# Kernel tuning notes

Measured on AMD Instinct MI355X. Metric: run time of the kernel, lower is better.

The kernel has to match this reference:

```python
import jax, jax.numpy as jnp
import numpy as np

HIDDEN = 51
N, T = 1024, 2048


def _uinit(key, shape, fan):
    bound = 1.0 / np.sqrt(fan)
    return jax.random.uniform(key, shape, jnp.float32, -bound, bound)


def setup_inputs() -> dict:
    key = jax.random.key(0)
    ks = jax.random.split(key, 9)
    H = HIDDEN
    return {
        "stimulus": jax.random.normal(ks[0], (N, T), jnp.float32),
        # layer 1: LSTMCell(input=1, hidden=H); torch gate order [i, f, g, o]
        "W_ih1": _uinit(ks[1], (4 * H, 1), H),
        "W_hh1": _uinit(ks[2], (4 * H, H), H),
        "b_ih1": _uinit(ks[3], (4 * H,), H),
        "b_hh1": _uinit(ks[4], (4 * H,), H),
        # layer 2: LSTMCell(input=H, hidden=1)
        "W_ih2": _uinit(ks[5], (4, H), 1),
        "W_hh2": _uinit(ks[6], (4, 1), 1),
        "b_ih2": _uinit(ks[7], (4,), 1),
        "b_hh2": _uinit(ks[8], (4,), 1),
    }


def _lstm_cell(x, h, c, W_ih, W_hh, b_ih, b_hh):
    # x: (N, in), h/c: (N, H). torch LSTMCell math, gate order i,f,g,o.
    gates = x @ W_ih.T + h @ W_hh.T + b_ih + b_hh  # (N, 4H)
    i, f, g, o = jnp.split(gates, 4, axis=-1)
    c_new = jax.nn.sigmoid(f) * c + jax.nn.sigmoid(i) * jnp.tanh(g)
    h_new = jax.nn.sigmoid(o) * jnp.tanh(c_new)
    return h_new, c_new


def reference(stimulus, W_ih1, W_hh1, b_ih1, b_hh1, W_ih2, W_hh2, b_ih2, b_hh2):
    n, t = stimulus.shape
    H = W_hh1.shape[1]
    h1 = jnp.zeros((n, H), stimulus.dtype)
    c1 = jnp.zeros((n, H), stimulus.dtype)
    h2 = jnp.zeros((n, 1), stimulus.dtype)
    c2 = jnp.zeros((n, 1), stimulus.dtype)

    def step(carry, x_t):  # x_t: (N,)
        h1, c1, h2, c2 = carry
        h1, c1 = _lstm_cell(x_t[:, None], h1, c1, W_ih1, W_hh1, b_ih1, b_hh1)
        h2, c2 = _lstm_cell(h1, h2, c2, W_ih2, W_hh2, b_ih2, b_hh2)
        return (h1, c1, h2, c2), h2[:, 0]

    _, ys = jax.lax.scan(step, (h1, c1, h2, c2), stimulus.T)  # ys: (T, N)
    return ys.T  # (N, T)
```

## Files before the change

### kernel.cpp

```cpp
#include <hip/hip_runtime.h>


constexpr int H  = 51;
constexpr int TL = 2048;

typedef float v2f __attribute__((ext_vector_type(2)));

__device__ __forceinline__ float rcpf(float x)   { return __builtin_amdgcn_rcpf(x); }
__device__ __forceinline__ float exp2f_(float x) { return __builtin_amdgcn_exp2f(x); }

constexpr float LOG2E  = 1.442695041f;
constexpr float LOG2E2 = 2.885390082f;

template <int CTRL>
__device__ __forceinline__ float dppmov(float v) {
    return __int_as_float(__builtin_amdgcn_update_dpp(
        0, __float_as_int(v), CTRL, 0xF, 0xF, true));
}

__device__ __forceinline__ float wave_sum(float p) {
    p += dppmov<0xB1>(p);
    p += dppmov<0x4E>(p);
    p += dppmov<0x124>(p);
    p += dppmov<0x128>(p);
    p += __int_as_float(__builtin_amdgcn_ds_swizzle(__float_as_int(p), 0x401f));
    p += __shfl_xor(p, 32, 64);
    return p;
}

template <int PAT>
__device__ __forceinline__ float quadb(float v) {
    return __int_as_float(__builtin_amdgcn_update_dpp(
        0, __float_as_int(v), PAT, 0xF, 0xF, true));
}

__device__ __forceinline__ void pk_fma(v2f& acc, const v2f a, const v2f b) {
    asm("v_pk_fma_f32 %0, %1, %2, %0" : "+v"(acc) : "v"(a), "v"(b));
}

__device__ __forceinline__ void layer2_step(
    const float* __restrict__ hprev, int lane,
    const float4& w2, const float4& wh2, const float4& b2,
    float* __restrict__ c2h2, float* __restrict__ out_ptr)
{
    const float hp = (lane < H) ? hprev[lane] : 0.0f;
    const float p0 = wave_sum(w2.x * hp);
    const float p1 = wave_sum(w2.y * hp);
    const float p2 = wave_sum(w2.z * hp);
    const float p3 = wave_sum(w2.w * hp);
    const float c2 = c2h2[0], h2 = c2h2[1];
    const float a0 = fmaf(wh2.x, h2, p0) + b2.x;
    const float a1 = fmaf(wh2.y, h2, p1) + b2.y;
    const float a2 = fmaf(wh2.z, h2, p2) + b2.z;
    const float a3 = fmaf(wh2.w, h2, p3) + b2.w;
    const float si = rcpf(1.0f + exp2f_(a0 * -LOG2E));
    const float sf = rcpf(1.0f + exp2f_(a1 * -LOG2E));
    const float tg = 1.0f - 2.0f * rcpf(1.0f + exp2f_(a2 * LOG2E2));
    const float so = rcpf(1.0f + exp2f_(a3 * -LOG2E));
    const float c2n = fmaf(sf, c2, si * tg);
    const float h2n = so * (1.0f - 2.0f * rcpf(1.0f + exp2f_(c2n * LOG2E2)));
    if (lane == 0) { c2h2[0] = c2n; c2h2[1] = h2n; *out_ptr = h2n; }
}

__global__ void
__attribute__((amdgpu_flat_work_group_size(256, 256)))
__attribute__((amdgpu_waves_per_eu(4, 4)))
lstm2_fused(const float* __restrict__ stim,
            const float* __restrict__ Wih1,
            const float* __restrict__ Whh1,
            const float* __restrict__ bih1,
            const float* __restrict__ bhh1,
            const float* __restrict__ Wih2,
            const float* __restrict__ Whh2,
            const float* __restrict__ bih2,
            const float* __restrict__ bhh2,
            float* __restrict__ out)
{
    const int n    = blockIdx.x;
    const int tid  = threadIdx.x;
    const int wid  = tid >> 6;
    const int lane = tid & 63;
    const int gate = lane & 3;
    const int unit = wid * 16 + (lane >> 2);
    const bool uval = (unit < H);

    __shared__ __align__(16) float xrow[TL];
    __shared__ __align__(16) float hbuf[2][56];
    __shared__ float c2h2[2];

    {
        const float4* s4 = reinterpret_cast<const float4*>(stim + (size_t)n * TL);
        float4* d4 = reinterpret_cast<float4*>(xrow);
        d4[tid]       = s4[tid];
        d4[tid + 256] = s4[tid + 256];
    }

    v2f wa0, wb0, wa1, wb1, wa2, wb2, wa3, wb3, wa4, wb4, wa5, wb5,
        wa6, wb6, wa7, wb7, wa8, wb8, wa9, wb9, wa10, wb10, wa11, wb11,
        wa12, wb12;
    float bsum = 0.0f, wi1 = 0.0f;
    {
        const v2f z = {0.0f, 0.0f};
        wa0=z; wb0=z; wa1=z; wb1=z; wa2=z; wb2=z; wa3=z; wb3=z; wa4=z; wb4=z;
        wa5=z; wb5=z; wa6=z; wb6=z; wa7=z; wb7=z; wa8=z; wb8=z; wa9=z; wb9=z;
        wa10=z; wb10=z; wa11=z; wb11=z; wa12=z; wb12=z;
    }
    if (uval) {
        const int r = gate * H + unit;
        const float* wr = Whh1 + r * H;
        #define LDJ(J) wa##J = (v2f){wr[4*(J)+0], wr[4*(J)+1]}; \
                       wb##J = (v2f){wr[4*(J)+2], wr[4*(J)+3]};
        LDJ(0) LDJ(1) LDJ(2) LDJ(3) LDJ(4) LDJ(5)
        LDJ(6) LDJ(7) LDJ(8) LDJ(9) LDJ(10) LDJ(11)
        #undef LDJ
        wa12 = (v2f){wr[48], wr[49]};
        wb12 = (v2f){wr[50], 0.0f};
        bsum = bih1[r] + bhh1[r];
        wi1  = Wih1[r];
    }

    float4 w2c, wh2c, b2c;
    w2c = make_float4(
        (lane < H) ? Wih2[0 * H + lane] : 0.0f,
        (lane < H) ? Wih2[1 * H + lane] : 0.0f,
        (lane < H) ? Wih2[2 * H + lane] : 0.0f,
        (lane < H) ? Wih2[3 * H + lane] : 0.0f);
    wh2c = make_float4(Whh2[0], Whh2[1], Whh2[2], Whh2[3]);
    b2c  = make_float4(bih2[0] + bhh2[0], bih2[1] + bhh2[1],
                       bih2[2] + bhh2[2], bih2[3] + bhh2[3]);

    if (tid < 56) { hbuf[0][tid] = 0.0f; hbuf[1][tid] = 0.0f; }
    if (tid == 0) { c2h2[0] = 0.0f; c2h2[1] = 0.0f; }
    __syncthreads();

    float c1 = 0.0f;
    float* out_row = out + (size_t)n * TL;
    const int rot = (n + (n >> 8)) & 3;

    for (int t = 0; t < TL; ++t) {
        const float* hprev = hbuf[(t & 1) ^ 1];

        if (t > 0 && wid == ((t + rot) & 3)) {
            layer2_step(hprev, lane, w2c, wh2c, b2c, c2h2, out_row + (t - 1));
        }

        const float x = xrow[t];
        v2f acc0 = {fmaf(x, wi1, bsum), 0.0f};
        v2f acc1 = {0.0f, 0.0f};
        const float4* h4 = reinterpret_cast<const float4*>(hprev);
        #define DOT(J) { const float4 hv = h4[J]; \
            pk_fma(acc0, wa##J, (v2f){hv.x, hv.y}); \
            pk_fma(acc1, wb##J, (v2f){hv.z, hv.w}); }
        DOT(0) DOT(1) DOT(2) DOT(3) DOT(4) DOT(5)
        DOT(6) DOT(7) DOT(8) DOT(9) DOT(10) DOT(11) DOT(12)
        #undef DOT
        const float a = (acc0.x + acc1.x) + (acc0.y + acc1.y);

        const bool  istanh = (gate == 2);
        const float k  = istanh ? LOG2E2 : -LOG2E;
        const float rr = rcpf(1.0f + exp2f_(a * k));
        const float v  = istanh ? fmaf(-2.0f, rr, 1.0f) : rr;

        const float vi = quadb<0x00>(v);
        const float vf = quadb<0x55>(v);
        const float vg = quadb<0xAA>(v);
        const float vo = quadb<0xFF>(v);

        c1 = fmaf(vf, c1, vi * vg);
        const float h1 = vo * (1.0f - 2.0f * rcpf(1.0f + exp2f_(c1 * LOG2E2)));
        if (uval && gate == 0) hbuf[t & 1][unit] = h1;

        __syncthreads();
    }

    if (wid == ((TL + rot) & 3)) {
        layer2_step(hbuf[(TL & 1) ^ 1], lane, w2c, wh2c, b2c, c2h2, out_row + (TL - 1));
    }
}

extern "C" void kernel_launch(void* const* d_in, const int* in_sizes, int n_in,
                              void* d_out, int out_size, void* d_ws, size_t ws_size,
                              hipStream_t stream) {
    const float* stim = (const float*)d_in[0];
    const float* Wih1 = (const float*)d_in[1];
    const float* Whh1 = (const float*)d_in[2];
    const float* bih1 = (const float*)d_in[3];
    const float* bhh1 = (const float*)d_in[4];
    const float* Wih2 = (const float*)d_in[5];
    const float* Whh2 = (const float*)d_in[6];
    const float* bih2 = (const float*)d_in[7];
    const float* bhh2 = (const float*)d_in[8];
    float* out = (float*)d_out;

    const int N = in_sizes[0] / TL;
    lstm2_fused<<<dim3(N), dim3(256), 0, stream>>>(
        stim, Wih1, Whh1, bih1, bhh1, Wih2, Whh2, bih2, bhh2, out);
}
```

Baseline: 1.745 ms.

## Split each gate dot product across two lanes and double block size to 512

Each block now uses 8 waves, and each (unit, gate) row's 51-element recurrent dot product is split across two adjacent lanes, which are combined with a DPP swap. This roughly halves the serial FMA chain per step. Gate values are gathered with ds_swizzle across 8-lane groups, and the layer-2 step rotates across 8 waves. The cost is more waves competing per barrier, fewer resident blocks per CU, and swizzle latency on the critical path.

After: 2.484 ms. 42.3% more time.

```diff
diff --git a/kernel.cpp b/kernel.cpp
--- a/kernel.cpp
+++ b/kernel.cpp
@@ -5,6 +5,7 @@
 constexpr int TL = 2048;
 
 typedef float v2f __attribute__((ext_vector_type(2)));
+typedef float v4f __attribute__((ext_vector_type(4)));
 
 __device__ __forceinline__ float rcpf(float x)   { return __builtin_amdgcn_rcpf(x); }
 __device__ __forceinline__ float exp2f_(float x) { return __builtin_amdgcn_exp2f(x); }
@@ -18,20 +19,19 @@
         0, __float_as_int(v), CTRL, 0xF, 0xF, true));
 }
 
+template <int OFF>
+__device__ __forceinline__ float swzb(float v) {
+    return __int_as_float(__builtin_amdgcn_ds_swizzle(__float_as_int(v), OFF));
+}
+
 __device__ __forceinline__ float wave_sum(float p) {
     p += dppmov<0xB1>(p);
     p += dppmov<0x4E>(p);
     p += dppmov<0x124>(p);
     p += dppmov<0x128>(p);
-    p += __int_as_float(__builtin_amdgcn_ds_swizzle(__float_as_int(p), 0x401f));
+    p += swzb<0x401f>(p);
     p += __shfl_xor(p, 32, 64);
     return p;
-}
-
-template <int PAT>
-__device__ __forceinline__ float quadb(float v) {
-    return __int_as_float(__builtin_amdgcn_update_dpp(
-        0, __float_as_int(v), PAT, 0xF, 0xF, true));
 }
 
 __device__ __forceinline__ void pk_fma(v2f& acc, const v2f a, const v2f b) {
@@ -62,27 +62,27 @@
     if (lane == 0) { c2h2[0] = c2n; c2h2[1] = h2n; *out_ptr = h2n; }
 }
 
-__global__ void
-__attribute__((amdgpu_flat_work_group_size(256, 256)))
-__attribute__((amdgpu_waves_per_eu(4, 4)))
-lstm2_fused(const float* __restrict__ stim,
-            const float* __restrict__ Wih1,
-            const float* __restrict__ Whh1,
-            const float* __restrict__ bih1,
-            const float* __restrict__ bhh1,
-            const float* __restrict__ Wih2,
-            const float* __restrict__ Whh2,
-            const float* __restrict__ bih2,
-            const float* __restrict__ bhh2,
-            float* __restrict__ out)
+__global__ __launch_bounds__(512)
+void lstm2_fused(const float* __restrict__ stim,
+                 const float* __restrict__ Wih1,
+                 const float* __restrict__ Whh1,
+                 const float* __restrict__ bih1,
+                 const float* __restrict__ bhh1,
+                 const float* __restrict__ Wih2,
+                 const float* __restrict__ Whh2,
+                 const float* __restrict__ bih2,
+                 const float* __restrict__ bhh2,
+                 float* __restrict__ out)
 {
     const int n    = blockIdx.x;
     const int tid  = threadIdx.x;
     const int wid  = tid >> 6;
     const int lane = tid & 63;
-    const int gate = lane & 3;
-    const int unit = wid * 16 + (lane >> 2);
+    const int half = lane & 1;
+    const int gate = (lane >> 1) & 3;
+    const int unit = wid * 8 + (lane >> 3);
     const bool uval = (unit < H);
+    const int kb   = half * 28;
 
     __shared__ __align__(16) float xrow[TL];
     __shared__ __align__(16) float hbuf[2][56];
@@ -91,43 +91,31 @@
     {
         const float4* s4 = reinterpret_cast<const float4*>(stim + (size_t)n * TL);
         float4* d4 = reinterpret_cast<float4*>(xrow);
-        d4[tid]       = s4[tid];
-        d4[tid + 256] = s4[tid + 256];
+        d4[tid] = s4[tid];
     }
 
-    v2f wa0, wb0, wa1, wb1, wa2, wb2, wa3, wb3, wa4, wb4, wa5, wb5,
-        wa6, wb6, wa7, wb7, wa8, wb8, wa9, wb9, wa10, wb10, wa11, wb11,
-        wa12, wb12;
-    float bsum = 0.0f, wi1 = 0.0f;
-    {
-        const v2f z = {0.0f, 0.0f};
-        wa0=z; wb0=z; wa1=z; wb1=z; wa2=z; wb2=z; wa3=z; wb3=z; wa4=z; wb4=z;
-        wa5=z; wb5=z; wa6=z; wb6=z; wa7=z; wb7=z; wa8=z; wb8=z; wa9=z; wb9=z;
-        wa10=z; wb10=z; wa11=z; wb11=z; wa12=z; wb12=z;
-    }
-    if (uval) {
-        const int r = gate * H + unit;
-        const float* wr = Whh1 + r * H;
-        #define LDJ(J) wa##J = (v2f){wr[4*(J)+0], wr[4*(J)+1]}; \
-                       wb##J = (v2f){wr[4*(J)+2], wr[4*(J)+3]};
-        LDJ(0) LDJ(1) LDJ(2) LDJ(3) LDJ(4) LDJ(5)
-        LDJ(6) LDJ(7) LDJ(8) LDJ(9) LDJ(10) LDJ(11)
-        #undef LDJ
-        wa12 = (v2f){wr[48], wr[49]};
-        wb12 = (v2f){wr[50], 0.0f};
-        bsum = bih1[r] + bhh1[r];
-        wi1  = Wih1[r];
-    }
+    const int r = gate * H + unit;
+    const float* wr = Whh1 + (size_t)(uval ? r : 0) * H;
+    #define SELW(K) (((K) < H && uval) ? wr[((K) < H) ? (K) : 0] : 0.0f)
+    v2f wpa0, wpb0, wpa1, wpb1, wpa2, wpb2, wpa3, wpb3, wpa4, wpb4,
+        wpa5, wpb5, wpa6, wpb6;
+    #define LW(J) wpa##J = (v2f){SELW(kb+4*(J)+0), SELW(kb+4*(J)+1)}; \
+                  wpb##J = (v2f){SELW(kb+4*(J)+2), SELW(kb+4*(J)+3)};
+    LW(0) LW(1) LW(2) LW(3) LW(4) LW(5) LW(6)
+    #undef LW
+    #undef SELW
+    const float bsum = uval ? (bih1[r] + bhh1[r]) : 0.0f;
+    const float wi1  = uval ? Wih1[r] : 0.0f;
 
-    float4 w2c, wh2c, b2c;
-    w2c = make_float4(
-        (lane < H) ? Wih2[0 * H + lane] : 0.0f,
-        (lane < H) ? Wih2[1 * H + lane] : 0.0f,
-        (lane < H) ? Wih2[2 * H + lane] : 0.0f,
-        (lane < H) ? Wih2[3 * H + lane] : 0.0f);
-    wh2c = make_float4(Whh2[0], Whh2[1], Whh2[2], Whh2[3]);
-    b2c  = make_float4(bih2[0] + bhh2[0], bih2[1] + bhh2[1],
-                       bih2[2] + bhh2[2], bih2[3] + bhh2[3]);
+    const int lc = (lane < H) ? lane : 0;
+    float4 w2c = make_float4(
+        (lane < H) ? Wih2[0 * H + lc] : 0.0f,
+        (lane < H) ? Wih2[1 * H + lc] : 0.0f,
+        (lane < H) ? Wih2[2 * H + lc] : 0.0f,
+        (lane < H) ? Wih2[3 * H + lc] : 0.0f);
+    float4 wh2c = make_float4(Whh2[0], Whh2[1], Whh2[2], Whh2[3]);
+    float4 b2c  = make_float4(bih2[0] + bhh2[0], bih2[1] + bhh2[1],
+                              bih2[2] + bhh2[2], bih2[3] + bhh2[3]);
 
     if (tid < 56) { hbuf[0][tid] = 0.0f; hbuf[1][tid] = 0.0f; }
     if (tid == 0) { c2h2[0] = 0.0f; c2h2[1] = 0.0f; }
@@ -135,45 +123,48 @@
 
     float c1 = 0.0f;
     float* out_row = out + (size_t)n * TL;
-    const int rot = (n + (n >> 8)) & 3;
+    const int rot = (n + (n >> 8)) & 7;
 
     for (int t = 0; t < TL; ++t) {
         const float* hprev = hbuf[(t & 1) ^ 1];
 
-        if (t > 0 && wid == ((t + rot) & 3)) {
+        if (t > 0 && wid == ((t + rot) & 7)) {
             layer2_step(hprev, lane, w2c, wh2c, b2c, c2h2, out_row + (t - 1));
         }
 
         const float x = xrow[t];
-        v2f acc0 = {fmaf(x, wi1, bsum), 0.0f};
+        const float* hp = hprev + kb;
+        v2f acc0 = {0.0f, 0.0f};
         v2f acc1 = {0.0f, 0.0f};
-        const float4* h4 = reinterpret_cast<const float4*>(hprev);
-        #define DOT(J) { const float4 hv = h4[J]; \
-            pk_fma(acc0, wa##J, (v2f){hv.x, hv.y}); \
-            pk_fma(acc1, wb##J, (v2f){hv.z, hv.w}); }
-        DOT(0) DOT(1) DOT(2) DOT(3) DOT(4) DOT(5)
-        DOT(6) DOT(7) DOT(8) DOT(9) DOT(10) DOT(11) DOT(12)
+        #define DOT(J) { const v4f hv = *reinterpret_cast<const v4f*>(hp + 4*(J)); \
+            const v2f lo = __builtin_shufflevector(hv, hv, 0, 1); \
+            const v2f hi = __builtin_shufflevector(hv, hv, 2, 3); \
+            pk_fma(acc0, wpa##J, lo); pk_fma(acc1, wpb##J, hi); }
+        DOT(0) DOT(1) DOT(2) DOT(3) DOT(4) DOT(5) DOT(6)
         #undef DOT
-        const float a = (acc0.x + acc1.x) + (acc0.y + acc1.y);
+        float apart = (acc0.x + acc1.x) + (acc0.y + acc1.y);
+        apart += dppmov<0xB1>(apart);
+        const float a = apart + fmaf(x, wi1, bsum);
 
         const bool  istanh = (gate == 2);
-        const float k  = istanh ? LOG2E2 : -LOG2E;
-        const float rr = rcpf(1.0f + exp2f_(a * k));
+        const float kk = istanh ? LOG2E2 : -LOG2E;
+        const float rr = rcpf(1.0f + exp2f_(a * kk));
         const float v  = istanh ? fmaf(-2.0f, rr, 1.0f) : rr;
 
-        const float vi = quadb<0x00>(v);
-        const float vf = quadb<0x55>(v);
-        const float vg = quadb<0xAA>(v);
-        const float vo = quadb<0xFF>(v);
+        const float vi = swzb<0x018>(v);
+        const float vf = swzb<0x058>(v);
+        const float vg = swzb<0x098>(v);
+        const float vo = swzb<0x0D8>(v);
 
         c1 = fmaf(vf, c1, vi * vg);
-        const float h1 = vo * (1.0f - 2.0f * rcpf(1.0f + exp2f_(c1 * LOG2E2)));
-        if (uval && gate == 0) hbuf[t & 1][unit] = h1;
+        const float tr = rcpf(1.0f + exp2f_(c1 * LOG2E2));
+        const float h1 = vo * fmaf(-2.0f, tr, 1.0f);
+        if (uval && (lane & 7) == 0) hbuf[t & 1][unit] = h1;
 
         __syncthreads();
     }
 
-    if (wid == ((TL + rot) & 3)) {
+    if (wid == ((TL + rot) & 7)) {
         layer2_step(hbuf[(TL & 1) ^ 1], lane, w2c, wh2c, b2c, c2h2, out_row + (TL - 1));
     }
 }
@@ -193,6 +184,6 @@
     float* out = (float*)d_out;
 
     const int N = in_sizes[0] / TL;
-    lstm2_fused<<<dim3(N), dim3(256), 0, stream>>>(
+    lstm2_fused<<<dim3(N), dim3(512), 0, stream>>>(
         stim, Wih1, Whh1, bih1, bhh1, Wih2, Whh2, bih2, bhh2, out);
 }
```

## Process four sequences per block with LDS-resident weights shared across sequences

Applied to the files above, without the earlier changes.

Each block now advances four batch rows together, holding W_hh1 in LDS (padded stride 52) instead of registers, so each weight load feeds four dot products. The grid shrinks to N/4 blocks and the per-step barrier is paid once for four sequences. Layer-2 state moves from shared memory into registers, with each wave handling layer 2 for its own sequence every step. The cost is roughly four times the serial work per step per block, more LDS traffic and usage, and far fewer blocks (256) to spread across the GPU.

Result: slower. 2.996 ms (+71.7%).

```diff
diff --git a/kernel.cpp b/kernel.cpp
--- a/kernel.cpp
+++ b/kernel.cpp
@@ -3,8 +3,11 @@
 
 constexpr int H  = 51;
 constexpr int TL = 2048;
+constexpr int R  = 4;
+constexpr int WS = 52;
 
 typedef float v2f __attribute__((ext_vector_type(2)));
+typedef float v4f __attribute__((ext_vector_type(4)));
 
 __device__ __forceinline__ float rcpf(float x)   { return __builtin_amdgcn_rcpf(x); }
 __device__ __forceinline__ float exp2f_(float x) { return __builtin_amdgcn_exp2f(x); }
@@ -16,6 +19,11 @@
 __device__ __forceinline__ float dppmov(float v) {
     return __int_as_float(__builtin_amdgcn_update_dpp(
         0, __float_as_int(v), CTRL, 0xF, 0xF, true));
+}
+
+template <int OFF>
+__device__ __forceinline__ float swzb(float v) {
+    return __int_as_float(__builtin_amdgcn_ds_swizzle(__float_as_int(v), OFF));
 }
 
 __device__ __forceinline__ float wave_sum(float p) {
@@ -23,7 +31,7 @@
     p += dppmov<0x4E>(p);
     p += dppmov<0x124>(p);
     p += dppmov<0x128>(p);
-    p += __int_as_float(__builtin_amdgcn_ds_swizzle(__float_as_int(p), 0x401f));
+    p += swzb<0x401f>(p);
     p += __shfl_xor(p, 32, 64);
     return p;
 }
@@ -39,32 +47,31 @@
 }
 
 __device__ __forceinline__ void layer2_step(
-    const float* __restrict__ hprev, int lane,
+    const float* __restrict__ hpm, int lane,
     const float4& w2, const float4& wh2, const float4& b2,
-    float* __restrict__ c2h2, float* __restrict__ out_ptr)
+    float& c2r, float& h2r, float* __restrict__ out_ptr)
 {
-    const float hp = (lane < H) ? hprev[lane] : 0.0f;
-    const float p0 = wave_sum(w2.x * hp);
-    const float p1 = wave_sum(w2.y * hp);
-    const float p2 = wave_sum(w2.z * hp);
-    const float p3 = wave_sum(w2.w * hp);
-    const float c2 = c2h2[0], h2 = c2h2[1];
-    const float a0 = fmaf(wh2.x, h2, p0) + b2.x;
-    const float a1 = fmaf(wh2.y, h2, p1) + b2.y;
-    const float a2 = fmaf(wh2.z, h2, p2) + b2.z;
-    const float a3 = fmaf(wh2.w, h2, p3) + b2.w;
+    const float hpv = (lane < H) ? hpm[lane] : 0.0f;
+    const float p0 = wave_sum(w2.x * hpv);
+    const float p1 = wave_sum(w2.y * hpv);
+    const float p2 = wave_sum(w2.z * hpv);
+    const float p3 = wave_sum(w2.w * hpv);
+    const float a0 = fmaf(wh2.x, h2r, p0) + b2.x;
+    const float a1 = fmaf(wh2.y, h2r, p1) + b2.y;
+    const float a2 = fmaf(wh2.z, h2r, p2) + b2.z;
+    const float a3 = fmaf(wh2.w, h2r, p3) + b2.w;
     const float si = rcpf(1.0f + exp2f_(a0 * -LOG2E));
     const float sf = rcpf(1.0f + exp2f_(a1 * -LOG2E));
     const float tg = 1.0f - 2.0f * rcpf(1.0f + exp2f_(a2 * LOG2E2));
     const float so = rcpf(1.0f + exp2f_(a3 * -LOG2E));
-    const float c2n = fmaf(sf, c2, si * tg);
-    const float h2n = so * (1.0f - 2.0f * rcpf(1.0f + exp2f_(c2n * LOG2E2)));
-    if (lane == 0) { c2h2[0] = c2n; c2h2[1] = h2n; *out_ptr = h2n; }
+    c2r = fmaf(sf, c2r, si * tg);
+    h2r = so * (1.0f - 2.0f * rcpf(1.0f + exp2f_(c2r * LOG2E2)));
+    if (lane == 0) *out_ptr = h2r;
 }
 
 __global__ void
 __attribute__((amdgpu_flat_work_group_size(256, 256)))
-__attribute__((amdgpu_waves_per_eu(4, 4)))
+__attribute__((amdgpu_waves_per_eu(1)))
 lstm2_fused(const float* __restrict__ stim,
             const float* __restrict__ Wih1,
             const float* __restrict__ Whh1,
@@ -76,106 +83,122 @@
             const float* __restrict__ bhh2,
             float* __restrict__ out)
 {
-    const int n    = blockIdx.x;
+    const int b    = blockIdx.x;
     const int tid  = threadIdx.x;
     const int wid  = tid >> 6;
     const int lane = tid & 63;
     const int gate = lane & 3;
     const int unit = wid * 16 + (lane >> 2);
     const bool uval = (unit < H);
-
-    __shared__ __align__(16) float xrow[TL];
-    __shared__ __align__(16) float hbuf[2][56];
-    __shared__ float c2h2[2];
-
-    {
-        const float4* s4 = reinterpret_cast<const float4*>(stim + (size_t)n * TL);
-        float4* d4 = reinterpret_cast<float4*>(xrow);
-        d4[tid]       = s4[tid];
-        d4[tid + 256] = s4[tid + 256];
+    const int r    = gate * H + unit;
+    const int rs   = uval ? r : 0;
+
+    __shared__ __align__(16) float wlds[204 * WS];
+    __shared__ __align__(16) float xrt[TL][R];
+    __shared__ __align__(16) float hb[2][R][WS];
+
+    for (int m = 0; m < R; ++m) {
+        const float4* s4 = reinterpret_cast<const float4*>(stim + (size_t)(b * R + m) * TL);
+        for (int i = tid; i < TL / 4; i += 256) {
+            const float4 v = s4[i];
+            xrt[4 * i + 0][m] = v.x;
+            xrt[4 * i + 1][m] = v.y;
+            xrt[4 * i + 2][m] = v.z;
+            xrt[4 * i + 3][m] = v.w;
+        }
     }
-
-    v2f wa0, wb0, wa1, wb1, wa2, wb2, wa3, wb3, wa4, wb4, wa5, wb5,
-        wa6, wb6, wa7, wb7, wa8, wb8, wa9, wb9, wa10, wb10, wa11, wb11,
-        wa12, wb12;
-    float bsum = 0.0f, wi1 = 0.0f;
-    {
-        const v2f z = {0.0f, 0.0f};
-        wa0=z; wb0=z; wa1=z; wb1=z; wa2=z; wb2=z; wa3=z; wb3=z; wa4=z; wb4=z;
-        wa5=z; wb5=z; wa6=z; wb6=z; wa7=z; wb7=z; wa8=z; wb8=z; wa9=z; wb9=z;
-        wa10=z; wb10=z; wa11=z; wb11=z; wa12=z; wb12=z;
+    for (int i = tid; i < 204 * H; i += 256) {
+        const int rr = i / H;
+        const int kk = i - rr * H;
+        wlds[rr * WS + kk] = Whh1[i];
     }
-    if (uval) {
-        const int r = gate * H + unit;
-        const float* wr = Whh1 + r * H;
-        #define LDJ(J) wa##J = (v2f){wr[4*(J)+0], wr[4*(J)+1]}; \
-                       wb##J = (v2f){wr[4*(J)+2], wr[4*(J)+3]};
-        LDJ(0) LDJ(1) LDJ(2) LDJ(3) LDJ(4) LDJ(5)
-        LDJ(6) LDJ(7) LDJ(8) LDJ(9) LDJ(10) LDJ(11)
-        #undef LDJ
-        wa12 = (v2f){wr[48], wr[49]};
-        wb12 = (v2f){wr[50], 0.0f};
-        bsum = bih1[r] + bhh1[r];
-        wi1  = Wih1[r];
-    }
-
-    float4 w2c, wh2c, b2c;
-    w2c = make_float4(
+    for (int i = tid; i < 204; i += 256) wlds[i * WS + H] = 0.0f;
+    for (int i = tid; i < 2 * R * WS; i += 256) (&hb[0][0][0])[i] = 0.0f;
+
+    const float bsum = uval ? (bih1[r] + bhh1[r]) : 0.0f;
+    const float wi1  = uval ? Wih1[r] : 0.0f;
+
+    float4 w2c = make_float4(
         (lane < H) ? Wih2[0 * H + lane] : 0.0f,
         (lane < H) ? Wih2[1 * H + lane] : 0.0f,
         (lane < H) ? Wih2[2 * H + lane] : 0.0f,
         (lane < H) ? Wih2[3 * H + lane] : 0.0f);
-    wh2c = make_float4(Whh2[0], Whh2[1], Whh2[2], Whh2[3]);
-    b2c  = make_float4(bih2[0] + bhh2[0], bih2[1] + bhh2[1],
-                       bih2[2] + bhh2[2], bih2[3] + bhh2[3]);
-
-    if (tid < 56) { hbuf[0][tid] = 0.0f; hbuf[1][tid] = 0.0f; }
-    if (tid == 0) { c2h2[0] = 0.0f; c2h2[1] = 0.0f; }
+    float4 wh2c = make_float4(Whh2[0], Whh2[1], Whh2[2], Whh2[3]);
+    float4 b2c  = make_float4(bih2[0] + bhh2[0], bih2[1] + bhh2[1],
+                              bih2[2] + bhh2[2], bih2[3] + bhh2[3]);
+
+    float c2r = 0.0f, h2r = 0.0f;
+    float* out_row = out + (size_t)(b * R + wid) * TL;
+
+    float c1_0 = 0.0f, c1_1 = 0.0f, c1_2 = 0.0f, c1_3 = 0.0f;
+    const float* wrow = wlds + rs * WS;
+
     __syncthreads();
 
-    float c1 = 0.0f;
-    float* out_row = out + (size_t)n * TL;
-    const int rot = (n + (n >> 8)) & 3;
-
     for (int t = 0; t < TL; ++t) {
-        const float* hprev = hbuf[(t & 1) ^ 1];
-
-        if (t > 0 && wid == ((t + rot) & 3)) {
-            layer2_step(hprev, lane, w2c, wh2c, b2c, c2h2, out_row + (t - 1));
+        const int pe = (t & 1) ^ 1;
+        const float* hp0 = &hb[pe][0][0];
+        const float* hp1 = &hb[pe][1][0];
+        const float* hp2 = &hb[pe][2][0];
+        const float* hp3 = &hb[pe][3][0];
+
+        if (t > 0) {
+            layer2_step(&hb[pe][wid][0], lane, w2c, wh2c, b2c, c2r, h2r,
+                        out_row + (t - 1));
         }
 
-        const float x = xrow[t];
-        v2f acc0 = {fmaf(x, wi1, bsum), 0.0f};
-        v2f acc1 = {0.0f, 0.0f};
-        const float4* h4 = reinterpret_cast<const float4*>(hprev);
-        #define DOT(J) { const float4 hv = h4[J]; \
-            pk_fma(acc0, wa##J, (v2f){hv.x, hv.y}); \
-            pk_fma(acc1, wb##J, (v2f){hv.z, hv.w}); }
-        DOT(0) DOT(1) DOT(2) DOT(3) DOT(4) DOT(5)
-        DOT(6) DOT(7) DOT(8) DOT(9) DOT(10) DOT(11) DOT(12)
-        #undef DOT
-        const float a = (acc0.x + acc1.x) + (acc0.y + acc1.y);
+        v2f a00 = {0,0}, a01 = {0,0}, a10 = {0,0}, a11 = {0,0};
+        v2f a20 = {0,0}, a21 = {0,0}, a30 = {0,0}, a31 = {0,0};
+        #define DOTJ(J) { \
+            const v4f wv = *reinterpret_cast<const v4f*>(wrow + 4*(J)); \
+            const v2f wlo = __builtin_shufflevector(wv, wv, 0, 1); \
+            const v2f whi = __builtin_shufflevector(wv, wv, 2, 3); \
+            const v4f h0v = *reinterpret_cast<const v4f*>(hp0 + 4*(J)); \
+            const v4f h1v = *reinterpret_cast<const v4f*>(hp1 + 4*(J)); \
+            const v4f h2v = *reinterpret_cast<const v4f*>(hp2 + 4*(J)); \
+            const v4f h3v = *reinterpret_cast<const v4f*>(hp3 + 4*(J)); \
+            pk_fma(a00, wlo, __builtin_shufflevector(h0v, h0v, 0, 1)); \
+            pk_fma(a01, whi, __builtin_shufflevector(h0v, h0v, 2, 3)); \
+            pk_fma(a10, wlo, __builtin_shufflevector(h1v, h1v, 0, 1)); \
+            pk_fma(a11, whi, __builtin_shufflevector(h1v, h1v, 2, 3)); \
+            pk_fma(a20, wlo, __builtin_shufflevector(h2v, h2v, 0, 1)); \
+            pk_fma(a21, whi, __builtin_shufflevector(h2v, h2v, 2, 3)); \
+            pk_fma(a30, wlo, __builtin_shufflevector(h3v, h3v, 0, 1)); \
+            pk_fma(a31, whi, __builtin_shufflevector(h3v, h3v, 2, 3)); }
+        DOTJ(0) DOTJ(1) DOTJ(2) DOTJ(3) DOTJ(4) DOTJ(5) DOTJ(6)
+        DOTJ(7) DOTJ(8) DOTJ(9) DOTJ(10) DOTJ(11) DOTJ(12)
+        #undef DOTJ
+
+        const v4f xv = *reinterpret_cast<const v4f*>(&xrt[t][0]);
+        const float aa0 = (a00.x + a00.y) + (a01.x + a01.y) + fmaf(xv.x, wi1, bsum);
+        const float aa1 = (a10.x + a10.y) + (a11.x + a11.y) + fmaf(xv.y, wi1, bsum);
+        const float aa2 = (a20.x + a20.y) + (a21.x + a21.y) + fmaf(xv.z, wi1, bsum);
+        const float aa3 = (a30.x + a30.y) + (a31.x + a31.y) + fmaf(xv.w, wi1, bsum);
 
         const bool  istanh = (gate == 2);
-        const float k  = istanh ? LOG2E2 : -LOG2E;
-        const float rr = rcpf(1.0f + exp2f_(a * k));
-        const float v  = istanh ? fmaf(-2.0f, rr, 1.0f) : rr;
-
-        const float vi = quadb<0x00>(v);
-        const float vf = quadb<0x55>(v);
-        const float vg = quadb<0xAA>(v);
-        const float vo = quadb<0xFF>(v);
-
-        c1 = fmaf(vf, c1, vi * vg);
-        const float h1 = vo * (1.0f - 2.0f * rcpf(1.0f + exp2f_(c1 * LOG2E2)));
-        if (uval && gate == 0) hbuf[t & 1][unit] = h1;
+        const float kk2 = istanh ? LOG2E2 : -LOG2E;
+        #define ACT(AA, C1, MIDX) { \
+            const float rr_ = rcpf(1.0f + exp2f_((AA) * kk2)); \
+            const float vv  = istanh ? fmaf(-2.0f, rr_, 1.0f) : rr_; \
+            const float vi = quadb<0x00>(vv); \
+            const float vf = quadb<0x55>(vv); \
+            const float vg = quadb<0xAA>(vv); \
+            const float vo = quadb<0xFF>(vv); \
+            C1 = fmaf(vf, C1, vi * vg); \
+            const float tr = rcpf(1.0f + exp2f_((C1) * LOG2E2)); \
+            const float h1v = vo * fmaf(-2.0f, tr, 1.0f); \
+            if (uval && gate == 0) hb[t & 1][MIDX][unit] = h1v; }
+        ACT(aa0, c1_0, 0)
+        ACT(aa1, c1_1, 1)
+        ACT(aa2, c1_2, 2)
+        ACT(aa3, c1_3, 3)
+        #undef ACT
 
         __syncthreads();
     }
 
-    if (wid == ((TL + rot) & 3)) {
-        layer2_step(hbuf[(TL & 1) ^ 1], lane, w2c, wh2c, b2c, c2h2, out_row + (TL - 1));
-    }
+    layer2_step(&hb[(TL & 1) ^ 1][wid][0], lane, w2c, wh2c, b2c, c2r, h2r,
+                out_row + (TL - 1));
 }
 
 extern "C" void kernel_launch(void* const* d_in, const int* in_sizes, int n_in,
@@ -193,6 +216,6 @@
     float* out = (float*)d_out;
 
     const int N = in_sizes[0] / TL;
-    lstm2_fused<<<dim3(N), dim3(256), 0, stream>>>(
+    lstm2_fused<<<dim3(N / R), dim3(256), 0, stream>>>(
         stim, Wih1, Whh1, bih1, bhh1, Wih2, Whh2, bih2, bhh2, out);
 }
```
